# Kernel optimization log

Measured on AMD Instinct MI355X. Metric: run time of the kernel, lower is better.

Reference implementation:

```python
import jax, jax.numpy as jnp
import numpy as np

N_WIRES = 4
N_LAYERS = 2
BSZ = 4096


def _gate(p):
    # combined single-qubit gate RX(p2) @ RZ(p1) @ RY(p0)  (RY applied first)
    a, b, c = p[0] * 0.5, p[1] * 0.5, p[2] * 0.5
    ca, sa = jnp.cos(a), jnp.sin(a)
    ry = jnp.stack([jnp.stack([ca, -sa]), jnp.stack([sa, ca])]).astype(jnp.complex64)
    eb = (jnp.cos(b) - 1j * jnp.sin(b)).astype(jnp.complex64)  # e^{-i b}
    zero = jnp.zeros((), jnp.complex64)
    rz = jnp.stack([jnp.stack([eb, zero]), jnp.stack([zero, jnp.conj(eb)])])
    cc, sc = jnp.cos(c), jnp.sin(c)
    rx = jnp.stack([jnp.stack([cc + 0j, -1j * sc]), jnp.stack([-1j * sc, cc + 0j])]).astype(jnp.complex64)
    return rx @ rz @ ry


def _apply1(state, U, w):
    # state: (N,2,2,2,2); apply 2x2 gate U on wire w
    s = jnp.moveaxis(state, w + 1, 4)
    s = jnp.einsum('nijka,ba->nijkb', s, U)
    return jnp.moveaxis(s, 4, w + 1)


def _cnot(state, c, t):
    s = jnp.moveaxis(state, (c + 1, t + 1), (1, 2))
    s = jnp.stack([s[:, 0], jnp.flip(s[:, 1], axis=1)], axis=1)
    return jnp.moveaxis(s, (1, 2), (c + 1, t + 1))


def _quanv(x, params):
    bsz = x.shape[0]
    # extract 2x2 patches in the same order as the torch loop:
    # [x[r,c], x[r,c+1], x[r+1,c], x[r+1,c+1]], row-major over (r,c)
    p = x.reshape(bsz, 14, 2, 14, 2).transpose(0, 1, 3, 2, 4).reshape(bsz * 196, 4)
    h = p * 0.5
    v = jnp.stack([jnp.cos(h), jnp.sin(h)], axis=-1).astype(jnp.complex64)  # (N,4,2): RY(patch)|0>
    state = jnp.einsum('na,nb,nc,nd->nabcd', v[:, 0], v[:, 1], v[:, 2], v[:, 3])
    for l in range(N_LAYERS):
        for w in range(N_WIRES):
            state = _apply1(state, _gate(params[l, w]), w)
        for w in range(N_WIRES - 1):
            state = _cnot(state, w, w + 1)
        state = _cnot(state, N_WIRES - 1, 0)
    probs = state.real ** 2 + state.imag ** 2  # (N,2,2,2,2)
    z = jnp.array([1.0, -1.0], jnp.float32)
    exps = []
    for w in range(N_WIRES):
        axes = tuple(i for i in range(1, 5) if i != w + 1)
        exps.append(probs.sum(axes) @ z)  # <Z_w>, shape (N,)
    # (N,4) -> (bsz, 196, 4) -> (bsz, 784), patch-major / wire-minor like torch.cat
    return jnp.stack(exps, axis=-1).reshape(bsz, 196 * N_WIRES)


def setup_inputs() -> dict:
    key = jax.random.key(0)
    k1, k2 = jax.random.split(key)
    x = jax.random.uniform(k1, (BSZ, 28, 28), dtype=jnp.float32)
    params = jax.random.normal(k2, (N_LAYERS, N_WIRES, 3), dtype=jnp.float32)
    return {"x": x, "params": params}


def reference(x, params):
    return _quanv(x, params)
```

## Files before the change

kernel.cpp:

```cpp
#include <hip/hip_runtime.h>


typedef _Float16 f16;
typedef _Float16 half8 __attribute__((ext_vector_type(8)));
typedef float f4 __attribute__((ext_vector_type(4)));

#define PK2(a, b) __builtin_bit_cast(float, __builtin_amdgcn_cvt_pkrtz((a), (b)))

__device__ __forceinline__ float2 cmulf(float2 a, float2 b) {
    return make_float2(fmaf(a.x, b.x, -(a.y * b.y)),
                       fmaf(a.x, b.y,   a.y * b.x));
}

__global__ __launch_bounds__(256, 4) void quanv_kernel(
        const float* __restrict__ x,
        const float* __restrict__ params,
        float* __restrict__ out)
{
    __shared__ float4 Gs[8];
    __shared__ __align__(16) f16 Wt[32][40];
    __shared__ __align__(16) unsigned char SB[4][5120];

    const int t = threadIdx.x;
    const int gid = blockIdx.x * 256 + t;

    const int n = gid / 196;
    const int p = gid - n * 196;
    const int r = p / 14;
    const int c = p - r * 14;
    const float* xb = x + n * 784 + r * 56 + c * 2;
    const float2 top = *(const float2*)(xb);
    const float2 bot = *(const float2*)(xb + 28);

    if (t < 8) {
        const float* pg = params + t * 3;
        const float ha = 0.5f * pg[0], hb = 0.5f * pg[1], hc = 0.5f * pg[2];
        const float sa = __sinf(ha), ca = __cosf(ha);
        const float sb = __sinf(hb), cb = __cosf(hb);
        const float sc = __sinf(hc), cx = __cosf(hc);
        Gs[t] = make_float4(cx*ca*cb + sc*sa*sb,
                            -(cx*ca*sb + sc*sa*cb),
                            sc*ca*sb - cx*sa*cb,
                            cx*sa*sb - sc*ca*cb);
    }
    __syncthreads();

    {
        const unsigned long long IDX1P = 0x497a2f1c85b6e3d0ULL;
        const unsigned long long INV1P = 0xa3185ce7d46f2b90ULL;
        const int iE = t >> 4;
        const int mE = t & 15;
        const int jN = (int)((IDX1P >> (iE * 4)) & 15);
        const int kN = (int)((INV1P >> (mE * 4)) & 15);
        float2 e = make_float2(1.f, 0.f);
#pragma unroll
        for (int w = 0; w < 4; ++w) {
            const float4 g = Gs[4 + w];
            const int jb = (jN >> (3 - w)) & 1;
            const int kb = (kN >> (3 - w)) & 1;
            const float ux = jb ? (kb ?  g.x : -g.z) : (kb ? g.z : g.x);
            const float uy = jb ? (kb ? -g.y :  g.w) : (kb ? g.w : g.y);
            e = cmulf(e, make_float2(ux, uy));
        }
        *(float*)&Wt[iE][2 * mE]      = PK2(e.x, -e.y);
        *(float*)&Wt[16 + iE][2 * mE] = PK2(e.y,  e.x);
    }

    const float pwv[4] = {0.5f * top.x, 0.5f * top.y, 0.5f * bot.x, 0.5f * bot.y};
    float2 wv[4][2];
#pragma unroll
    for (int w = 0; w < 4; ++w) {
        const float cw = __cosf(pwv[w]);
        const float sw = __sinf(pwv[w]);
        const float4 g = Gs[w];
        wv[w][0] = make_float2(fmaf(g.z, sw,  g.x * cw), fmaf( g.w, sw, g.y * cw));
        wv[w][1] = make_float2(fmaf(g.x, sw, -g.z * cw), fmaf(-g.y, sw, g.w * cw));
    }

    float2 ab[4], cd[4];
#pragma unroll
    for (int i = 0; i < 2; ++i)
#pragma unroll
        for (int j = 0; j < 2; ++j) {
            ab[i * 2 + j] = cmulf(wv[0][i], wv[1][j]);
            cd[i * 2 + j] = cmulf(wv[2][i], wv[3][j]);
        }
    float sd[16];
#pragma unroll
    for (int hi = 0; hi < 4; ++hi)
#pragma unroll
        for (int lo = 0; lo < 4; ++lo) {
            const float2 sv = cmulf(ab[hi], cd[lo]);
            sd[hi * 4 + lo] = PK2(sv.x, sv.y);
        }

    const int l   = t & 63;
    const int wid = t >> 6;
    const int q   = l >> 4;
    const int c16 = l & 15;

    f16* st = (f16*)(SB[wid] + l * 80);
    *(float4*)(st)      = make_float4(sd[0],  sd[1],  sd[2],  sd[3]);
    *(float4*)(st + 8)  = make_float4(sd[4],  sd[5],  sd[6],  sd[7]);
    *(float4*)(st + 16) = make_float4(sd[8],  sd[9],  sd[10], sd[11]);
    *(float4*)(st + 24) = make_float4(sd[12], sd[13], sd[14], sd[15]);

    __syncthreads();

    const half8 b0 = *(const half8*)&Wt[c16][q * 8];
    const half8 b1 = *(const half8*)&Wt[16 + c16][q * 8];
    const f4 zf4 = {0.f, 0.f, 0.f, 0.f};
    f4 d0[4], d1[4];
#pragma unroll
    for (int m = 0; m < 4; ++m) {
        const half8 am = *(const half8*)(SB[wid] + (m * 16 + c16) * 80 + q * 16);
        d0[m] = __builtin_amdgcn_mfma_f32_16x16x32_f16(am, b0, zf4, 0, 0, 0);
        d1[m] = __builtin_amdgcn_mfma_f32_16x16x32_f16(am, b1, zf4, 0, 0, 0);
    }

    float* prb = (float*)SB[wid];
#pragma unroll
    for (int m = 0; m < 4; ++m)
#pragma unroll
        for (int reg = 0; reg < 4; ++reg) {
            const float pv = fmaf(d0[m][reg], d0[m][reg], d1[m][reg] * d1[m][reg]);
            prb[(m * 16 + q * 4 + reg) * 20 + c16] = pv;
        }

    const float4 p0 = *(const float4*)(prb + l * 20);
    const float4 p1 = *(const float4*)(prb + l * 20 + 4);
    const float4 p2 = *(const float4*)(prb + l * 20 + 8);
    const float4 p3 = *(const float4*)(prb + l * 20 + 12);

    const float t00 = p0.x + p0.y + p0.z + p0.w;
    const float t01 = p1.x + p1.y + p1.z + p1.w;
    const float t10 = p2.x + p2.y + p2.z + p2.w;
    const float t11 = p3.x + p3.y + p3.z + p3.w;
    const float e0 = (t00 + t01) - (t10 + t11);
    const float e1 = (t00 - t01) + (t10 - t11);

    const float u00 = p0.x + p1.x + p2.x + p3.x;
    const float u01 = p0.y + p1.y + p2.y + p3.y;
    const float u10 = p0.z + p1.z + p2.z + p3.z;
    const float u11 = p0.w + p1.w + p2.w + p3.w;
    const float e2 = (u00 + u01) - (u10 + u11);
    const float e3 = (u00 - u01) + (u10 - u11);

    *(float4*)(out + gid * 4) = make_float4(e0, e1, e2, e3);
}

extern "C" void kernel_launch(void* const* d_in, const int* in_sizes, int n_in,
                              void* d_out, int out_size, void* d_ws, size_t ws_size,
                              hipStream_t stream) {
    const float* x      = (const float*)d_in[0];
    const float* params = (const float*)d_in[1];
    float* out = (float*)d_out;

    const int npatch = 4096 * 196;
    quanv_kernel<<<npatch / 256, 256, 0, stream>>>(x, params, out);
}
```

Measured before the change: 72.66 us.

## Precompute full circuit unitary in a setup kernel and feed real product state to MFMA

A tiny pre-kernel now folds both layers' gates into one 16x16 complex matrix (layer-1 single-qubit gates times the layer-2 map) and writes it to workspace as f16. The main kernel drops its per-block gate setup, its shared-memory weight table and its __syncthreads. Since the input state is a real product of cos/sin terms, it builds 16 real amplitudes and zeros the imaginary half of the MFMA A operand. It also raises occupancy to 6 blocks per CU. The cost is an extra kernel launch, and more of the gate product is rounded to f16, which may hurt accuracy.

After: 71.42 us. Within noise of the previous version (-1.7%).

```diff
diff --git a/kernel.cpp b/kernel.cpp
--- a/kernel.cpp
+++ b/kernel.cpp
@@ -12,13 +12,63 @@
                        fmaf(a.x, b.y,   a.y * b.x));
 }
 
-__global__ __launch_bounds__(256, 4) void quanv_kernel(
+__global__ void build_w_kernel(const float* __restrict__ params,
+                               f16* __restrict__ wg) {
+    __shared__ float4 Gs[8];
+    const int t = threadIdx.x;
+    if (t < 8) {
+        const float* pg = params + t * 3;
+        const float ha = 0.5f * pg[0], hb = 0.5f * pg[1], hc = 0.5f * pg[2];
+        const float sa = __sinf(ha), ca = __cosf(ha);
+        const float sb = __sinf(hb), cb = __cosf(hb);
+        const float sc = __sinf(hc), cx = __cosf(hc);
+        Gs[t] = make_float4(cx*ca*cb + sc*sa*sb,
+                            -(cx*ca*sb + sc*sa*cb),
+                            sc*ca*sb - cx*sa*cb,
+                            cx*sa*sb - sc*ca*cb);
+    }
+    __syncthreads();
+
+    const unsigned long long IDX1P = 0x497a2f1c85b6e3d0ULL;
+    const unsigned long long INV1P = 0xa3185ce7d46f2b90ULL;
+    const int i = t >> 4;
+    const int m = t & 15;
+    const int jN = (int)((IDX1P >> (i * 4)) & 15);
+    float accx = 0.f, accy = 0.f;
+    for (int k = 0; k < 16; ++k) {
+        const int kN = (int)((INV1P >> (k * 4)) & 15);
+        float2 a = make_float2(1.f, 0.f);
+        float2 b = make_float2(1.f, 0.f);
+#pragma unroll
+        for (int w = 0; w < 4; ++w) {
+            const float4 g2 = Gs[4 + w];
+            const int jb = (jN >> (3 - w)) & 1;
+            const int kb = (kN >> (3 - w)) & 1;
+            const float ux = jb ? (kb ?  g2.x : -g2.z) : (kb ? g2.z : g2.x);
+            const float uy = jb ? (kb ? -g2.y :  g2.w) : (kb ? g2.w : g2.y);
+            a = cmulf(a, make_float2(ux, uy));
+            const float4 g1 = Gs[w];
+            const int kb1 = (k >> (3 - w)) & 1;
+            const int mb  = (m >> (3 - w)) & 1;
+            const float vx = kb1 ? (mb ?  g1.x : -g1.z) : (mb ? g1.z : g1.x);
+            const float vy = kb1 ? (mb ? -g1.y :  g1.w) : (mb ? g1.w : g1.y);
+            b = cmulf(b, make_float2(vx, vy));
+        }
+        const float2 ab = cmulf(a, b);
+        accx += ab.x;
+        accy += ab.y;
+    }
+    wg[i * 32 + m]             = (f16)accx;
+    wg[i * 32 + 16 + m]        = (f16)0.f;
+    wg[(16 + i) * 32 + m]      = (f16)accy;
+    wg[(16 + i) * 32 + 16 + m] = (f16)0.f;
+}
+
+__global__ __launch_bounds__(256, 6) void quanv_kernel(
         const float* __restrict__ x,
-        const float* __restrict__ params,
+        const f16*   __restrict__ wg,
         float* __restrict__ out)
 {
-    __shared__ float4 Gs[8];
-    __shared__ __align__(16) f16 Wt[32][40];
     __shared__ __align__(16) unsigned char SB[4][5120];
 
     const int t = threadIdx.x;
@@ -32,99 +82,48 @@
     const float2 top = *(const float2*)(xb);
     const float2 bot = *(const float2*)(xb + 28);
 
-    if (t < 8) {
-        const float* pg = params + t * 3;
-        const float ha = 0.5f * pg[0], hb = 0.5f * pg[1], hc = 0.5f * pg[2];
-        const float sa = __sinf(ha), ca = __cosf(ha);
-        const float sb = __sinf(hb), cb = __cosf(hb);
-        const float sc = __sinf(hc), cx = __cosf(hc);
-        Gs[t] = make_float4(cx*ca*cb + sc*sa*sb,
-                            -(cx*ca*sb + sc*sa*cb),
-                            sc*ca*sb - cx*sa*cb,
-                            cx*sa*sb - sc*ca*cb);
-    }
-    __syncthreads();
-
-    {
-        const unsigned long long IDX1P = 0x497a2f1c85b6e3d0ULL;
-        const unsigned long long INV1P = 0xa3185ce7d46f2b90ULL;
-        const int iE = t >> 4;
-        const int mE = t & 15;
-        const int jN = (int)((IDX1P >> (iE * 4)) & 15);
-        const int kN = (int)((INV1P >> (mE * 4)) & 15);
-        float2 e = make_float2(1.f, 0.f);
-#pragma unroll
-        for (int w = 0; w < 4; ++w) {
-            const float4 g = Gs[4 + w];
-            const int jb = (jN >> (3 - w)) & 1;
-            const int kb = (kN >> (3 - w)) & 1;
-            const float ux = jb ? (kb ?  g.x : -g.z) : (kb ? g.z : g.x);
-            const float uy = jb ? (kb ? -g.y :  g.w) : (kb ? g.w : g.y);
-            e = cmulf(e, make_float2(ux, uy));
-        }
-        *(float*)&Wt[iE][2 * mE]      = PK2(e.x, -e.y);
-        *(float*)&Wt[16 + iE][2 * mE] = PK2(e.y,  e.x);
-    }
-
-    const float pwv[4] = {0.5f * top.x, 0.5f * top.y, 0.5f * bot.x, 0.5f * bot.y};
-    float2 wv[4][2];
-#pragma unroll
-    for (int w = 0; w < 4; ++w) {
-        const float cw = __cosf(pwv[w]);
-        const float sw = __sinf(pwv[w]);
-        const float4 g = Gs[w];
-        wv[w][0] = make_float2(fmaf(g.z, sw,  g.x * cw), fmaf( g.w, sw, g.y * cw));
-        wv[w][1] = make_float2(fmaf(g.x, sw, -g.z * cw), fmaf(-g.y, sw, g.w * cw));
-    }
-
-    float2 ab[4], cd[4];
-#pragma unroll
-    for (int i = 0; i < 2; ++i)
-#pragma unroll
-        for (int j = 0; j < 2; ++j) {
-            ab[i * 2 + j] = cmulf(wv[0][i], wv[1][j]);
-            cd[i * 2 + j] = cmulf(wv[2][i], wv[3][j]);
-        }
-    float sd[16];
-#pragma unroll
-    for (int hi = 0; hi < 4; ++hi)
-#pragma unroll
-        for (int lo = 0; lo < 4; ++lo) {
-            const float2 sv = cmulf(ab[hi], cd[lo]);
-            sd[hi * 4 + lo] = PK2(sv.x, sv.y);
-        }
-
     const int l   = t & 63;
     const int wid = t >> 6;
     const int q   = l >> 4;
     const int c16 = l & 15;
 
+    const half8 b0 = *(const half8*)(wg + c16 * 32 + q * 8);
+    const half8 b1 = *(const half8*)(wg + (16 + c16) * 32 + q * 8);
+
+    const float h0 = 0.5f * top.x, h1 = 0.5f * top.y;
+    const float h2 = 0.5f * bot.x, h3 = 0.5f * bot.y;
+    const float c0 = __cosf(h0), s0 = __sinf(h0);
+    const float c1 = __cosf(h1), s1 = __sinf(h1);
+    const float c2 = __cosf(h2), s2 = __sinf(h2);
+    const float c3 = __cosf(h3), s3 = __sinf(h3);
+    const float A0 = c0 * c1, A1 = c0 * s1, A2 = s0 * c1, A3 = s0 * s1;
+    const float B0 = c2 * c3, B1 = c2 * s3, B2 = s2 * c3, B3 = s2 * s3;
+
     f16* st = (f16*)(SB[wid] + l * 80);
-    *(float4*)(st)      = make_float4(sd[0],  sd[1],  sd[2],  sd[3]);
-    *(float4*)(st + 8)  = make_float4(sd[4],  sd[5],  sd[6],  sd[7]);
-    *(float4*)(st + 16) = make_float4(sd[8],  sd[9],  sd[10], sd[11]);
-    *(float4*)(st + 24) = make_float4(sd[12], sd[13], sd[14], sd[15]);
+    *(float4*)(st)      = make_float4(PK2(A0 * B0, A0 * B1), PK2(A0 * B2, A0 * B3),
+                                      PK2(A1 * B0, A1 * B1), PK2(A1 * B2, A1 * B3));
+    *(float4*)(st + 8)  = make_float4(PK2(A2 * B0, A2 * B1), PK2(A2 * B2, A2 * B3),
+                                      PK2(A3 * B0, A3 * B1), PK2(A3 * B2, A3 * B3));
+    const float4 zz = make_float4(0.f, 0.f, 0.f, 0.f);
+    *(float4*)(st + 16) = zz;
+    *(float4*)(st + 24) = zz;
 
-    __syncthreads();
-
-    const half8 b0 = *(const half8*)&Wt[c16][q * 8];
-    const half8 b1 = *(const half8*)&Wt[16 + c16][q * 8];
     const f4 zf4 = {0.f, 0.f, 0.f, 0.f};
     f4 d0[4], d1[4];
 #pragma unroll
-    for (int m = 0; m < 4; ++m) {
-        const half8 am = *(const half8*)(SB[wid] + (m * 16 + c16) * 80 + q * 16);
-        d0[m] = __builtin_amdgcn_mfma_f32_16x16x32_f16(am, b0, zf4, 0, 0, 0);
-        d1[m] = __builtin_amdgcn_mfma_f32_16x16x32_f16(am, b1, zf4, 0, 0, 0);
+    for (int mm = 0; mm < 4; ++mm) {
+        const half8 am = *(const half8*)(SB[wid] + (mm * 16 + c16) * 80 + q * 16);
+        d0[mm] = __builtin_amdgcn_mfma_f32_16x16x32_f16(am, b0, zf4, 0, 0, 0);
+        d1[mm] = __builtin_amdgcn_mfma_f32_16x16x32_f16(am, b1, zf4, 0, 0, 0);
     }
 
     float* prb = (float*)SB[wid];
 #pragma unroll
-    for (int m = 0; m < 4; ++m)
+    for (int mm = 0; mm < 4; ++mm)
 #pragma unroll
         for (int reg = 0; reg < 4; ++reg) {
-            const float pv = fmaf(d0[m][reg], d0[m][reg], d1[m][reg] * d1[m][reg]);
-            prb[(m * 16 + q * 4 + reg) * 20 + c16] = pv;
+            const float pv = fmaf(d0[mm][reg], d0[mm][reg], d1[mm][reg] * d1[mm][reg]);
+            prb[(mm * 16 + q * 4 + reg) * 20 + c16] = pv;
         }
 
     const float4 p0 = *(const float4*)(prb + l * 20);
@@ -155,7 +154,9 @@
     const float* x      = (const float*)d_in[0];
     const float* params = (const float*)d_in[1];
     float* out = (float*)d_out;
+    f16* wg = (f16*)d_ws;
 
+    build_w_kernel<<<1, 256, 0, stream>>>(params, wg);
     const int npatch = 4096 * 196;
-    quanv_kernel<<<npatch / 256, 256, 0, stream>>>(x, params, out);
+    quanv_kernel<<<npatch / 256, 256, 0, stream>>>(x, wg, out);
 }
```
